# Kernel optimization log

Hardware: AMD Instinct MI355X
Metric: run time of the kernel (lower is better)

Reference implementation:

```python
import jax, jax.numpy as jnp
import numpy as np

DIM = 384
WIN = 7
HEADS = 12
N = WIN * WIN
B_ = 4096
NW = 64


def _relative_position_index(ws: int) -> np.ndarray:
    coords = np.stack(np.meshgrid(np.arange(ws), np.arange(ws), indexing='ij'))  # (2, ws, ws)
    flat = coords.reshape(2, -1)  # (2, N)
    rel = flat[:, :, None] - flat[:, None, :]  # (2, N, N)
    rel = rel.transpose(1, 2, 0).copy()  # (N, N, 2)
    rel[:, :, 0] += ws - 1
    rel[:, :, 1] += ws - 1
    rel[:, :, 0] *= 2 * ws - 1
    return rel.sum(-1).astype(np.int32)  # (N, N)


def setup_inputs() -> dict:
    key = jax.random.key(0)
    ks = jax.random.split(key, 6)
    x = jax.random.normal(ks[0], (B_, N, DIM), dtype=jnp.float32)
    mask = jnp.zeros((NW, N, N), dtype=jnp.float32)
    bias_table = 0.02 * jax.random.normal(ks[1], ((2 * WIN - 1) ** 2, HEADS), dtype=jnp.float32)
    qkv_w = jax.random.normal(ks[2], (3 * DIM, DIM), dtype=jnp.float32) / np.sqrt(DIM)
    qkv_b = jnp.zeros((3 * DIM,), dtype=jnp.float32)
    proj_w = jax.random.normal(ks[3], (DIM, DIM), dtype=jnp.float32) / np.sqrt(DIM)
    proj_b = jnp.zeros((DIM,), dtype=jnp.float32)
    rel_index = jnp.asarray(_relative_position_index(WIN))  # (N, N) int32
    return {"x": x, "mask": mask, "bias_table": bias_table, "qkv_w": qkv_w,
            "qkv_b": qkv_b, "proj_w": proj_w, "proj_b": proj_b, "rel_index": rel_index}


def reference(x, mask, bias_table, qkv_w, qkv_b, proj_w, proj_b, rel_index):
    Bw, n, c = x.shape
    h = bias_table.shape[1]
    d = c // h
    scale = d ** (-0.5)
    # qkv projection: (Bw, n, 3, h, d)
    qkv = (x @ qkv_w.T + qkv_b).reshape(Bw, n, 3, h, d)
    qkv = jnp.transpose(qkv, (2, 0, 3, 1, 4))  # (3, Bw, h, n, d)
    q, k, v = qkv[0], qkv[1], qkv[2]
    attn = jnp.einsum('bhqd,bhkd->bhqk', q * scale, k)  # (Bw, h, n, n)
    bias = bias_table[rel_index]  # (n, n, h)
    attn = attn + jnp.transpose(bias, (2, 0, 1))[None]  # broadcast over Bw
    nW = mask.shape[0]
    attn = attn.reshape(Bw // nW, nW, h, n, n) + mask[None, :, None]
    attn = attn.reshape(Bw, h, n, n)
    attn = jax.nn.softmax(attn, axis=-1)
    out = jnp.einsum('bhqk,bhkd->bhqd', attn, v)  # (Bw, h, n, d)
    out = jnp.transpose(out, (0, 2, 1, 3)).reshape(Bw, n, c)
    return out @ proj_w.T + proj_b
```

## Files before the change

### kernel.cpp

```cpp
#include <hip/hip_runtime.h>
#include <hip/hip_bf16.h>

#define DIM   384
#define NWIN  49
#define HEADS 12
#define SCALE 0.17677669529663687f

typedef unsigned short ushort;
using bf16x8 = __attribute__((ext_vector_type(8))) short;
using u16x4  = __attribute__((ext_vector_type(4))) ushort;
using f32x4  = __attribute__((ext_vector_type(4))) float;

__device__ __forceinline__ ushort f2bf(float f) {
  unsigned u = __float_as_uint(f);
  u += 0x7fff + ((u >> 16) & 1);
  return (ushort)(u >> 16);
}

typedef __attribute__((address_space(1))) const void gas_void;
typedef __attribute__((address_space(3))) void las_void;

__device__ __forceinline__ void gload16(const ushort* g, ushort* l) {
  __builtin_amdgcn_global_load_lds((gas_void*)g, (las_void*)l, 16, 0, 0);
}

__global__ void prep_kernel(const float* __restrict__ qkv_w, const float* __restrict__ proj_w,
                            const float* __restrict__ bias_table, const int* __restrict__ rel_index,
                            const float* __restrict__ mask, const float* __restrict__ qkv_b,
                            ushort* __restrict__ wqb, ushort* __restrict__ wpb,
                            float* __restrict__ qbF, float* __restrict__ bmF) {
  int i0 = blockIdx.x * 256 + threadIdx.x;
  int stride = gridDim.x * 256;
  for (int i = i0; i < 1152 * 384; i += stride) {
    float v = qkv_w[i];
    if (i < 384 * 384) v *= SCALE;
    wqb[i] = f2bf(v);
  }
  for (int i = i0; i < 384 * 384; i += stride) wpb[i] = f2bf(proj_w[i]);
  for (int i = i0; i < 1152; i += stride) qbF[i] = qkv_b[i] * (i < 384 ? SCALE : 1.f);
  for (int i = i0; i < 64 * HEADS * 4 * 4 * 64 * 4; i += stride) {
    int r = i & 3, lane = (i >> 2) & 63, kt = (i >> 8) & 3, wq = (i >> 10) & 3;
    int hw = i >> 12;
    int h = hw % HEADS, wdx = hw / HEADS;
    int q = wq * 16 + (lane >> 4) * 4 + r;
    int key = kt * 16 + (lane & 15);
    float v;
    if (q < NWIN)
      v = (key < NWIN) ? bias_table[rel_index[q * NWIN + key] * HEADS + h]
                         + mask[wdx * (NWIN * NWIN) + q * NWIN + key]
                       : -3.0e38f;
    else
      v = 0.f;
    bmF[i] = v;
  }
}

__global__ __launch_bounds__(256) void x2bf_kernel(const float* __restrict__ x,
                                                   ushort* __restrict__ xbf) {
  size_t i = (size_t)blockIdx.x * 256 + threadIdx.x;
  float4 f = ((const float4*)x)[i];
  u16x4 v4 = { f2bf(f.x), f2bf(f.y), f2bf(f.z), f2bf(f.w) };
  ((u16x4*)xbf)[i] = v4;
}

__global__ __launch_bounds__(256) void qkv_gemm_bf16_kernel(
    const ushort* __restrict__ xbf, const float* __restrict__ qbF,
    const ushort* __restrict__ wqb,
    ushort* __restrict__ qg, ushort* __restrict__ kg, ushort* __restrict__ vg)
{
  extern __shared__ ushort smA[];
  ushort* lA = smA;
  ushort* lB = smA + 16384;

  const int hw = blockIdx.x;
  const int xcd = hw & 7, slot = hw >> 3;
  const int pan = slot / 9, bN = slot - pan * 9;
  const int bM = (pan << 3) + xcd;
  const int m0 = bM * 128, n0 = bN * 128;
  const int which = bN / 3;
  ushort* outw = which == 0 ? qg : (which == 1 ? kg : vg);
  const int tid = threadIdx.x;
  const int w = tid >> 6, l = tid & 63;
  const int c = l & 15, g = l >> 4;
  const int wm = w >> 1, wn = w & 1;

  auto stageA = [&](int kc, int buf) {
    #pragma unroll
    for (int s = 0; s < 4; ++s) {
      int i = s * 256 + tid;
      int row = i >> 3, gc = i & 7;
      bf16x8 vx = *(const bf16x8*)(xbf + (size_t)(m0 + row) * DIM + kc * 64 + gc * 8);
      *(bf16x8*)&lA[buf * 8192 + row * 64 + ((gc ^ (row & 7)) << 3)] = vx;
    }
  };
  auto stageB = [&](int kc, int buf) {
    #pragma unroll
    for (int s = 0; s < 4; ++s) {
      int i = s * 256 + tid;
      int row = i >> 3, gc = i & 7;
      gload16(wqb + (size_t)(n0 + row) * DIM + kc * 64 + ((gc ^ (row & 7)) << 3),
              lB + buf * 8192 + i * 8);
    }
  };

  f32x4 acc[4][4] = {};
  stageA(0, 0); stageB(0, 0);
  stageA(1, 1); stageB(1, 1);
  __syncthreads();

  for (int kc = 0; kc < 6; ++kc) {
    const ushort* A = lA + (kc & 1) * 8192;
    const ushort* B = lB + (kc & 1) * 8192;
    #pragma unroll
    for (int kk = 0; kk < 2; ++kk) {
      int swz = ((kk * 4 + g) ^ (c & 7)) << 3;
      bf16x8 af[4], bfr[4];
      #pragma unroll
      for (int mt = 0; mt < 4; ++mt)
        af[mt] = *(const bf16x8*)&A[(wm * 64 + mt * 16 + c) * 64 + swz];
      #pragma unroll
      for (int nt = 0; nt < 4; ++nt)
        bfr[nt] = *(const bf16x8*)&B[(wn * 64 + nt * 16 + c) * 64 + swz];
      #pragma unroll
      for (int mt = 0; mt < 4; ++mt)
        #pragma unroll
        for (int nt = 0; nt < 4; ++nt)
          acc[mt][nt] = __builtin_amdgcn_mfma_f32_16x16x32_bf16(af[mt], bfr[nt], acc[mt][nt], 0, 0, 0);
    }
    __syncthreads();
    if (kc + 2 < 6) { stageA(kc + 2, kc & 1); stageB(kc + 2, kc & 1); }
  }

  #pragma unroll
  for (int nt = 0; nt < 4; ++nt) {
    int n = n0 + wn * 64 + nt * 16 + c;
    int h = (n - which * 384) >> 5;
    int d = n & 31;
    float qb_ = qbF[n];
    #pragma unroll
    for (int mt = 0; mt < 4; ++mt) {
      #pragma unroll
      for (int r = 0; r < 4; ++r) {
        int tok = m0 + wm * 64 + mt * 16 + g * 4 + r;
        int win = tok / 49;
        int tk = tok - win * 49;
        outw[((size_t)(win * HEADS + h) * NWIN + tk) * 32 + d] = f2bf(acc[mt][nt][r] + qb_);
      }
    }
  }
}

__global__ __launch_bounds__(256) void qkv_gemm_kernel(
    const float* __restrict__ x, const float* __restrict__ qbF,
    const ushort* __restrict__ wqb,
    ushort* __restrict__ qg, ushort* __restrict__ kg, ushort* __restrict__ vg)
{
  extern __shared__ ushort smA[];
  ushort* lA = smA;
  ushort* lB = smA + 16384;

  const int hw = blockIdx.x;
  const int xcd = hw & 7, slot = hw >> 3;
  const int pan = slot / 9, bN = slot - pan * 9;
  const int bM = (pan << 3) + xcd;
  const int m0 = bM * 128, n0 = bN * 128;
  const int which = bN / 3;
  ushort* outw = which == 0 ? qg : (which == 1 ? kg : vg);
  const int tid = threadIdx.x;
  const int w = tid >> 6, l = tid & 63;
  const int c = l & 15, g = l >> 4;
  const int wm = w >> 1, wn = w & 1;

  auto stageA = [&](int kc, int buf) {
    #pragma unroll
    for (int s = 0; s < 4; ++s) {
      int i = s * 256 + tid;
      int row = i >> 3, gc = i & 7;
      const float4* src = (const float4*)(x + (size_t)(m0 + row) * DIM + kc * 64 + gc * 8);
      float4 f0 = src[0], f1 = src[1];
      ushort tmp[8] = { f2bf(f0.x), f2bf(f0.y), f2bf(f0.z), f2bf(f0.w),
                        f2bf(f1.x), f2bf(f1.y), f2bf(f1.z), f2bf(f1.w) };
      *(bf16x8*)&lA[buf * 8192 + row * 64 + ((gc ^ (row & 7)) << 3)] = *(bf16x8*)tmp;
    }
  };
  auto stageB = [&](int kc, int buf) {
    #pragma unroll
    for (int s = 0; s < 4; ++s) {
      int i = s * 256 + tid;
      int row = i >> 3, gc = i & 7;
      gload16(wqb + (size_t)(n0 + row) * DIM + kc * 64 + ((gc ^ (row & 7)) << 3),
              lB + buf * 8192 + i * 8);
    }
  };

  f32x4 acc[4][4] = {};
  stageA(0, 0); stageB(0, 0);
  stageA(1, 1); stageB(1, 1);
  __syncthreads();

  for (int kc = 0; kc < 6; ++kc) {
    const ushort* A = lA + (kc & 1) * 8192;
    const ushort* B = lB + (kc & 1) * 8192;
    #pragma unroll
    for (int kk = 0; kk < 2; ++kk) {
      int swz = ((kk * 4 + g) ^ (c & 7)) << 3;
      bf16x8 af[4], bfr[4];
      #pragma unroll
      for (int mt = 0; mt < 4; ++mt)
        af[mt] = *(const bf16x8*)&A[(wm * 64 + mt * 16 + c) * 64 + swz];
      #pragma unroll
      for (int nt = 0; nt < 4; ++nt)
        bfr[nt] = *(const bf16x8*)&B[(wn * 64 + nt * 16 + c) * 64 + swz];
      #pragma unroll
      for (int mt = 0; mt < 4; ++mt)
        #pragma unroll
        for (int nt = 0; nt < 4; ++nt)
          acc[mt][nt] = __builtin_amdgcn_mfma_f32_16x16x32_bf16(af[mt], bfr[nt], acc[mt][nt], 0, 0, 0);
    }
    __syncthreads();
    if (kc + 2 < 6) { stageA(kc + 2, kc & 1); stageB(kc + 2, kc & 1); }
  }

  #pragma unroll
  for (int nt = 0; nt < 4; ++nt) {
    int n = n0 + wn * 64 + nt * 16 + c;
    int h = (n - which * 384) >> 5;
    int d = n & 31;
    float qb_ = qbF[n];
    #pragma unroll
    for (int mt = 0; mt < 4; ++mt) {
      #pragma unroll
      for (int r = 0; r < 4; ++r) {
        int tok = m0 + wm * 64 + mt * 16 + g * 4 + r;
        int win = tok / 49;
        int tk = tok - win * 49;
        outw[((size_t)(win * HEADS + h) * NWIN + tk) * 32 + d] = f2bf(acc[mt][nt][r] + qb_);
      }
    }
  }
}

#define VSTR 68
__global__ __launch_bounds__(256) void attn_kernel(
    const ushort* __restrict__ kg, const ushort* __restrict__ vg,
    const float* __restrict__ bmF, ushort* __restrict__ qg)
{
  __shared__ ushort vts[4][32 * VSTR];
  __shared__ ushort pbs[4][16 * 36];

  const int tid = threadIdx.x;
  const int w = tid >> 6, l = tid & 63;
  const int c = l & 15, g = l >> 4;
  const int task = blockIdx.x * 4 + w;
  const int win = task / 12, h = task - win * 12;
  const int wdx = win & 63;
  const float LOG2E = 1.4426950408889634f;

  const size_t sb = (size_t)(win * HEADS + h) * (NWIN * 32);
  ushort* qslice = qg + sb;
  const ushort* kb = kg + sb;
  const ushort* vb = vg + sb;
  ushort* vt = vts[w];
  ushort* pb = pbs[w];

  bf16x8 qf[4], kf[4];
  #pragma unroll
  for (int t = 0; t < 4; ++t) {
    qf[t] = *(const bf16x8*)(qslice + (t * 16 + c) * 32 + g * 8);
    kf[t] = *(const bf16x8*)(kb + (t * 16 + c) * 32 + g * 8);
  }
  #pragma unroll
  for (int it = 0; it < 25; ++it) {
    int i = it * 64 + l;
    if (i < NWIN * 32) vt[(i & 31) * VSTR + (i >> 5)] = vb[i];
  }
  for (int i = l; i < 32 * 15; i += 64) {
    int d = i / 15, t = NWIN + (i - d * 15);
    vt[d * VSTR + t] = 0;
  }

  const float* bmBase = bmF + (size_t)((wdx * HEADS + h) * 4) * 1024 + l * 4;

  #pragma unroll
  for (int qt = 0; qt < 4; ++qt) {
    f32x4 sacc[4] = {};
    #pragma unroll
    for (int kt = 0; kt < 4; ++kt)
      sacc[kt] = __builtin_amdgcn_mfma_f32_16x16x32_bf16(qf[qt], kf[kt], sacc[kt], 0, 0, 0);
    const f32x4* bw4 = (const f32x4*)(bmBase + qt * 1024);
    float p[4][4];
    {
      f32x4 b0 = bw4[0], b1 = bw4[64], b2 = bw4[128], b3 = bw4[192];
      #pragma unroll
      for (int r = 0; r < 4; ++r) {
        float s0 = sacc[0][r] + b0[r], s1 = sacc[1][r] + b1[r];
        float s2 = sacc[2][r] + b2[r], s3 = sacc[3][r] + b3[r];
        float mx = fmaxf(fmaxf(s0, s1), fmaxf(s2, s3));
        mx = fmaxf(mx, __shfl_xor(mx, 1, 64));
        mx = fmaxf(mx, __shfl_xor(mx, 2, 64));
        mx = fmaxf(mx, __shfl_xor(mx, 4, 64));
        mx = fmaxf(mx, __shfl_xor(mx, 8, 64));
        float p0 = __builtin_exp2f((s0 - mx) * LOG2E);
        float p1 = __builtin_exp2f((s1 - mx) * LOG2E);
        float p2 = __builtin_exp2f((s2 - mx) * LOG2E);
        float p3 = __builtin_exp2f((s3 - mx) * LOG2E);
        float sum = p0 + p1 + p2 + p3;
        sum += __shfl_xor(sum, 1, 64);
        sum += __shfl_xor(sum, 2, 64);
        sum += __shfl_xor(sum, 4, 64);
        sum += __shfl_xor(sum, 8, 64);
        float inv = 1.0f / sum;
        p[0][r] = p0 * inv; p[1][r] = p1 * inv; p[2][r] = p2 * inv; p[3][r] = p3 * inv;
      }
    }
    f32x4 pacc[2] = {};
    #pragma unroll
    for (int kkh = 0; kkh < 2; ++kkh) {
      #pragma unroll
      for (int t = 0; t < 2; ++t) {
        int kt = kkh * 2 + t;
        #pragma unroll
        for (int r = 0; r < 4; ++r)
          pb[(g * 4 + r) * 36 + t * 16 + c] = f2bf(p[kt][r]);
      }
      bf16x8 ap = *(const bf16x8*)&pb[c * 36 + g * 8];
      #pragma unroll
      for (int dt = 0; dt < 2; ++dt) {
        bf16x8 bv = *(const bf16x8*)&vt[(dt * 16 + c) * VSTR + kkh * 32 + g * 8];
        pacc[dt] = __builtin_amdgcn_mfma_f32_16x16x32_bf16(ap, bv, pacc[dt], 0, 0, 0);
      }
    }
    #pragma unroll
    for (int dt = 0; dt < 2; ++dt) {
      #pragma unroll
      for (int rr = 0; rr < 4; ++rr) {
        int tok = qt * 16 + g * 4 + rr;
        if (tok < NWIN)
          qslice[tok * 32 + dt * 16 + c] = f2bf(pacc[dt][rr]);
      }
    }
  }
}

__global__ __launch_bounds__(256, 2) void proj_kernel(
    const ushort* __restrict__ ao, const ushort* __restrict__ wpb,
    const float* __restrict__ proj_b, float* __restrict__ out)
{
  extern __shared__ ushort sm3[];
  ushort* lA = sm3;
  ushort* lB = sm3 + 16384;

  const int hw = blockIdx.x;
  const int xcd = hw & 7, slot = hw >> 3;
  const int pan = slot / 3, bN = slot - pan * 3;
  const int bM = (pan << 3) + xcd;
  const int m0 = bM * 128, n0 = bN * 128;
  const int tid = threadIdx.x;
  const int w = tid >> 6, l = tid & 63;
  const int c = l & 15, g = l >> 4;
  const int wm = w >> 1, wn = w & 1;

  auto stageA = [&](int kc, int buf) {
    #pragma unroll
    for (int s = 0; s < 4; ++s) {
      int i = s * 256 + tid;
      int row = i >> 3, gc = i & 7;
      int tok = m0 + row;
      int win = tok / 49;
      int tk = tok - win * 49;
      int sg = gc ^ (row & 7);
      int kfull = kc * 64 + sg * 8;
      gload16(ao + ((size_t)(win * HEADS + (kfull >> 5)) * NWIN + tk) * 32 + (kfull & 31),
              lA + buf * 8192 + i * 8);
    }
  };
  auto stageB = [&](int kc, int buf) {
    #pragma unroll
    for (int s = 0; s < 4; ++s) {
      int i = s * 256 + tid;
      int row = i >> 3, gc = i & 7;
      gload16(wpb + (size_t)(n0 + row) * DIM + kc * 64 + ((gc ^ (row & 7)) << 3),
              lB + buf * 8192 + i * 8);
    }
  };

  f32x4 acc[4][4] = {};
  stageA(0, 0); stageB(0, 0);
  stageA(1, 1); stageB(1, 1);
  __syncthreads();

  for (int kc = 0; kc < 6; ++kc) {
    const ushort* A = lA + (kc & 1) * 8192;
    const ushort* B = lB + (kc & 1) * 8192;
    #pragma unroll
    for (int kk = 0; kk < 2; ++kk) {
      int swz = ((kk * 4 + g) ^ (c & 7)) << 3;
      bf16x8 af[4], bfr[4];
      #pragma unroll
      for (int mt = 0; mt < 4; ++mt)
        af[mt] = *(const bf16x8*)&A[(wm * 64 + mt * 16 + c) * 64 + swz];
      #pragma unroll
      for (int nt = 0; nt < 4; ++nt)
        bfr[nt] = *(const bf16x8*)&B[(wn * 64 + nt * 16 + c) * 64 + swz];
      #pragma unroll
      for (int mt = 0; mt < 4; ++mt)
        #pragma unroll
        for (int nt = 0; nt < 4; ++nt)
          acc[mt][nt] = __builtin_amdgcn_mfma_f32_16x16x32_bf16(af[mt], bfr[nt], acc[mt][nt], 0, 0, 0);
    }
    __syncthreads();
    if (kc + 2 < 6) { stageA(kc + 2, kc & 1); stageB(kc + 2, kc & 1); }
  }

  #pragma unroll
  for (int nt = 0; nt < 4; ++nt) {
    int col = n0 + wn * 64 + nt * 16 + c;
    float pb = proj_b[col];
    #pragma unroll
    for (int mt = 0; mt < 4; ++mt) {
      #pragma unroll
      for (int r = 0; r < 4; ++r) {
        int row = m0 + wm * 64 + mt * 16 + g * 4 + r;
        out[(size_t)row * DIM + col] = acc[mt][nt][r] + pb;
      }
    }
  }
}

#define FWB_OFF 0
#define FQS_OFF 24576
#define FKS_OFF 29696
#define FVT_OFF 34816
#define FAO_OFF 39424
#define FSMEM_US 77056

__global__ __launch_bounds__(512, 2) void winattn_fused(
    const float* __restrict__ x, const float* __restrict__ qbF,
    const float* __restrict__ proj_b, const ushort* __restrict__ wqb,
    const ushort* __restrict__ wpb, const float* __restrict__ bmF,
    float* __restrict__ out)
{
  extern __shared__ ushort smem[];
  ushort* wb = smem + FWB_OFF;
  ushort* ao = smem + FAO_OFF;

  const int blk = blockIdx.x;
  const int tid = threadIdx.x;
  const int w = tid >> 6, l = tid & 63;
  const int c = l & 15, g = l >> 4;
  const int wm = w >> 1, wn = w & 1;
  const int win = w >> 2, wq = w & 3;
  const float LOG2E = 1.4426950408889634f;

  ushort* qsw = smem + FQS_OFF + win * 2560;
  ushort* ksw = smem + FKS_OFF + win * 2560;
  ushort* vtw = smem + FVT_OFF + win * 2304;
  ushort* psw = qsw;

  auto stage_qkv = [&](int h, int kc, int buf) {
    #pragma unroll
    for (int s = 0; s < 3; ++s) {
      int i = s * 512 + tid;
      int n = i >> 4, g16 = i & 15;
      int grow = (n >> 5) * 384 + h * 32 + (n & 31);
      int sg = (g16 & 8) | ((g16 & 7) ^ (n & 7));
      gload16(wqb + (size_t)grow * DIM + kc * 128 + (sg << 3), wb + buf * 12288 + i * 8);
    }
  };
  auto stage_proj = [&](int nb, int kc, int buf) {
    #pragma unroll
    for (int s = 0; s < 3; ++s) {
      int i = s * 512 + tid;
      int n = i >> 4, g16 = i & 15;
      int grow = nb * 96 + n;
      int sg = (g16 & 8) | ((g16 & 7) ^ (n & 7));
      gload16(wpb + (size_t)grow * DIM + kc * 128 + (sg << 3), wb + buf * 12288 + i * 8);
    }
  };

  bf16x8 areg[2][12] = {};
  auto compute_qkv = [&](int kcC, int buf, f32x4 (&acc)[2][3]) {
    const ushort* wcb = wb + buf * 12288;
    #pragma unroll
    for (int kk = 0; kk < 4; ++kk) {
      int sB = ((kk * 4 + g) ^ (c & 7)) << 3;
      #pragma unroll
      for (int nt = 0; nt < 3; ++nt) {
        int n = (wn * 3 + nt) * 16 + c;
        bf16x8 bb = *(const bf16x8*)&wcb[n * 128 + sB];
        acc[0][nt] = __builtin_amdgcn_mfma_f32_16x16x32_bf16(areg[0][kcC * 4 + kk], bb, acc[0][nt], 0, 0, 0);
        acc[1][nt] = __builtin_amdgcn_mfma_f32_16x16x32_bf16(areg[1][kcC * 4 + kk], bb, acc[1][nt], 0, 0, 0);
      }
    }
  };
  auto compute_proj = [&](int kcC, int buf, f32x4 (&acc)[2][3]) {
    const ushort* wcb = wb + buf * 12288;
    int r0 = wm * 32 + c;      if (r0 >= 98) r0 -= 64;
    int r1 = wm * 32 + 16 + c; if (r1 >= 98) r1 -= 64;
    #pragma unroll
    for (int kk = 0; kk < 4; ++kk) {
      int p = kcC * 16 + kk * 4 + g;
      int sw = (p ^ (c & 7)) << 3;
      bf16x8 a0 = *(const bf16x8*)&ao[r0 * 384 + sw];
      bf16x8 a1 = *(const bf16x8*)&ao[r1 * 384 + sw];
      int sB = ((kk * 4 + g) ^ (c & 7)) << 3;
      #pragma unroll
      for (int nt = 0; nt < 3; ++nt) {
        int n = (wn * 3 + nt) * 16 + c;
        bf16x8 bb = *(const bf16x8*)&wcb[n * 128 + sB];
        acc[0][nt] = __builtin_amdgcn_mfma_f32_16x16x32_bf16(a0, bb, acc[0][nt], 0, 0, 0);
        acc[1][nt] = __builtin_amdgcn_mfma_f32_16x16x32_bf16(a1, bb, acc[1][nt], 0, 0, 0);
      }
    }
  };

  stage_qkv(0, 0, 0);
  stage_qkv(0, 1, 1);
  {
    const float* xb = x + (size_t)blk * (2 * NWIN * DIM);
    for (int i = tid; i < 9408; i += 512) {
      float4 f = ((const float4*)xb)[i];
      int row = i / 96, c4 = i - row * 96;
      int k = c4 * 4;
      int gr = k >> 3;
      u16x4 v4 = { f2bf(f.x), f2bf(f.y), f2bf(f.z), f2bf(f.w) };
      *(u16x4*)&ao[row * 384 + ((gr ^ (row & 7)) << 3) + (k & 7)] = v4;
    }
  }
  __syncthreads();
  #pragma unroll
  for (int mt = 0; mt < 2; ++mt) {
    int row = wm * 32 + mt * 16 + c;
    int wi = row >> 6, tok = row & 63;
    if (tok < NWIN) {
      int ar = wi * 49 + tok;
      #pragma unroll
      for (int kg = 0; kg < 12; ++kg)
        areg[mt][kg] = *(const bf16x8*)&ao[ar * 384 + (((kg * 4 + g) ^ (ar & 7)) << 3)];
    }
  }

  for (int h = 0; h < HEADS; ++h) {
    f32x4 acc[2][3] = {};
    const int par = h & 1;
    compute_qkv(0, par, acc);
    __syncthreads();
    stage_qkv(h, 2, par);
    compute_qkv(1, par ^ 1, acc);
    __syncthreads();
    if (h < 11) stage_qkv(h + 1, 0, par ^ 1); else stage_proj(0, 0, par ^ 1);
    compute_qkv(2, par, acc);
    __syncthreads();
    if (h < 11) stage_qkv(h + 1, 1, par); else stage_proj(0, 1, par);
    {
      int winE = wm >> 1;
      ushort* qsE = smem + FQS_OFF + winE * 2560;
      ushort* ksE = smem + FKS_OFF + winE * 2560;
      ushort* vtE = smem + FVT_OFF + winE * 2304;
      #pragma unroll
      for (int nt = 0; nt < 3; ++nt) {
        int gnt = wn * 3 + nt;
        int which = gnt >> 1;
        int d = (gnt & 1) * 16 + c;
        float qb_ = qbF[which * 384 + h * 32 + d];
        #pragma unroll
        for (int mt = 0; mt < 2; ++mt) {
          #pragma unroll
          for (int r = 0; r < 4; ++r) {
            int tok = (wm & 1) * 32 + mt * 16 + g * 4 + r;
            float v = acc[mt][nt][r] + qb_;
            if (which == 0)      qsE[tok * 40 + d] = f2bf(v);
            else if (which == 1) ksE[tok * 40 + d] = f2bf(v);
            else                 vtE[d * 72 + tok] = f2bf(v);
          }
        }
      }
    }
    __syncthreads();

    const int wdx = ((blk << 1) + win) & 63;
    const f32x4* bw4 = (const f32x4*)(bmF + ((((size_t)(wdx * HEADS + h)) * 4 + wq) * 4 * 64 + l) * 4);
    f32x4 bmv[4];
    #pragma unroll
    for (int kt = 0; kt < 4; ++kt) bmv[kt] = bw4[kt * 64];

    f32x4 sacc[4] = {};
    {
      bf16x8 aq = *(const bf16x8*)&qsw[(wq * 16 + c) * 40 + g * 8];
      #pragma unroll
      for (int kt = 0; kt < 4; ++kt) {
        bf16x8 bk = *(const bf16x8*)&ksw[(kt * 16 + c) * 40 + g * 8];
        sacc[kt] = __builtin_amdgcn_mfma_f32_16x16x32_bf16(aq, bk, sacc[kt], 0, 0, 0);
      }
    }
    float p[4][4];
    #pragma unroll
    for (int r = 0; r < 4; ++r) {
      float s0 = sacc[0][r] + bmv[0][r], s1 = sacc[1][r] + bmv[1][r];
      float s2 = sacc[2][r] + bmv[2][r], s3 = sacc[3][r] + bmv[3][r];
      float mx = fmaxf(fmaxf(s0, s1), fmaxf(s2, s3));
      mx = fmaxf(mx, __shfl_xor(mx, 1, 64));
      mx = fmaxf(mx, __shfl_xor(mx, 2, 64));
      mx = fmaxf(mx, __shfl_xor(mx, 4, 64));
      mx = fmaxf(mx, __shfl_xor(mx, 8, 64));
      float p0 = __builtin_exp2f((s0 - mx) * LOG2E);
      float p1 = __builtin_exp2f((s1 - mx) * LOG2E);
      float p2 = __builtin_exp2f((s2 - mx) * LOG2E);
      float p3 = __builtin_exp2f((s3 - mx) * LOG2E);
      float sum = p0 + p1 + p2 + p3;
      sum += __shfl_xor(sum, 1, 64);
      sum += __shfl_xor(sum, 2, 64);
      sum += __shfl_xor(sum, 4, 64);
      sum += __shfl_xor(sum, 8, 64);
      float inv = 1.0f / sum;
      p[0][r] = p0 * inv; p[1][r] = p1 * inv; p[2][r] = p2 * inv; p[3][r] = p3 * inv;
    }
    f32x4 pacc2[2] = {};
    #pragma unroll
    for (int kkh = 0; kkh < 2; ++kkh) {
      #pragma unroll
      for (int t = 0; t < 2; ++t) {
        int kt = kkh * 2 + t;
        #pragma unroll
        for (int r = 0; r < 4; ++r)
          psw[(wq * 16 + g * 4 + r) * 40 + t * 16 + c] = f2bf(p[kt][r]);
      }
      bf16x8 ap = *(const bf16x8*)&psw[(wq * 16 + c) * 40 + g * 8];
      #pragma unroll
      for (int dt = 0; dt < 2; ++dt) {
        bf16x8 bv = *(const bf16x8*)&vtw[(dt * 16 + c) * 72 + kkh * 32 + g * 8];
        pacc2[dt] = __builtin_amdgcn_mfma_f32_16x16x32_bf16(ap, bv, pacc2[dt], 0, 0, 0);
      }
    }
    #pragma unroll
    for (int dt = 0; dt < 2; ++dt) {
      int gr0 = h * 4 + dt * 2 + (c >> 3);
      #pragma unroll
      for (int rr = 0; rr < 4; ++rr) {
        int tok = wq * 16 + g * 4 + rr;
        int row0 = win * 49 + tok;
        if (tok < NWIN)
          ao[row0 * 384 + (((gr0 ^ (row0 & 7)) << 3) | (c & 7))] = f2bf(pacc2[dt][rr]);
      }
    }
    __syncthreads();
  }

  __syncthreads();
  for (int nb = 0; nb < 4; ++nb) {
    f32x4 acc[2][3] = {};
    const int pb0 = (nb * 3) & 1;
    compute_proj(0, pb0, acc);
    __syncthreads();
    stage_proj(nb, 2, pb0);
    compute_proj(1, pb0 ^ 1, acc);
    __syncthreads();
    if (nb < 3) stage_proj(nb + 1, 0, pb0 ^ 1);
    compute_proj(2, pb0, acc);
    __syncthreads();
    if (nb < 3) stage_proj(nb + 1, 1, pb0);
    #pragma unroll
    for (int nt = 0; nt < 3; ++nt) {
      int col = nb * 96 + (wn * 3 + nt) * 16 + c;
      float pb = proj_b[col];
      #pragma unroll
      for (int mt = 0; mt < 2; ++mt) {
        #pragma unroll
        for (int r = 0; r < 4; ++r) {
          int mrow = wm * 32 + mt * 16 + g * 4 + r;
          if (mrow < 98) {
            int wi = mrow >= NWIN;
            int tok = mrow - (wi ? NWIN : 0);
            out[((size_t)((blk << 1) + wi) * NWIN + tok) * DIM + col] = acc[mt][nt][r] + pb;
          }
        }
      }
    }
  }
}

extern "C" void kernel_launch(void* const* d_in, const int* in_sizes, int n_in,
                              void* d_out, int out_size, void* d_ws, size_t ws_size,
                              hipStream_t stream) {
  const float* x          = (const float*)d_in[0];
  const float* mask       = (const float*)d_in[1];
  const float* bias_table = (const float*)d_in[2];
  const float* qkv_w      = (const float*)d_in[3];
  const float* qkv_b      = (const float*)d_in[4];
  const float* proj_w     = (const float*)d_in[5];
  const float* proj_b     = (const float*)d_in[6];
  const int*   rel_index  = (const int*)d_in[7];
  float* out = (float*)d_out;

  ushort* wqb = (ushort*)d_ws;
  ushort* wpb = (ushort*)((char*)d_ws + 884736);
  float*  qbF = (float*)((char*)d_ws + 1179648);
  float*  bmF = (float*)((char*)d_ws + 1184256);
  ushort* qg  = (ushort*)((char*)d_ws + 13767168);
  ushort* kg  = (ushort*)((char*)d_ws + 167907840);
  ushort* vg  = (ushort*)((char*)d_ws + 322048512);
  ushort* xbf = (ushort*)((char*)d_ws + 476189184);
  const size_t NEED1 = 630329856ull;
  const size_t NEED2 = 476189184ull;

  prep_kernel<<<1024, 256, 0, stream>>>(qkv_w, proj_w, bias_table, rel_index, mask, qkv_b,
                                        wqb, wpb, qbF, bmF);

  if (ws_size >= NEED1) {
    x2bf_kernel<<<75264, 256, 0, stream>>>(x, xbf);
    hipFuncSetAttribute((const void*)qkv_gemm_bf16_kernel,
                        hipFuncAttributeMaxDynamicSharedMemorySize, 65536);
    qkv_gemm_bf16_kernel<<<14112, 256, 65536, stream>>>(xbf, qbF, wqb, qg, kg, vg);
    attn_kernel<<<12288, 256, 0, stream>>>(kg, vg, bmF, qg);
    hipFuncSetAttribute((const void*)proj_kernel,
                        hipFuncAttributeMaxDynamicSharedMemorySize, 65536);
    proj_kernel<<<4704, 256, 65536, stream>>>(qg, wpb, proj_b, out);
  } else if (ws_size >= NEED2) {
    hipFuncSetAttribute((const void*)qkv_gemm_kernel,
                        hipFuncAttributeMaxDynamicSharedMemorySize, 65536);
    qkv_gemm_kernel<<<14112, 256, 65536, stream>>>(x, qbF, wqb, qg, kg, vg);
    attn_kernel<<<12288, 256, 0, stream>>>(kg, vg, bmF, qg);
    hipFuncSetAttribute((const void*)proj_kernel,
                        hipFuncAttributeMaxDynamicSharedMemorySize, 65536);
    proj_kernel<<<4704, 256, 65536, stream>>>(qg, wpb, proj_b, out);
  } else {
    hipFuncSetAttribute((const void*)winattn_fused,
                        hipFuncAttributeMaxDynamicSharedMemorySize, FSMEM_US * 2);
    winattn_fused<<<2048, 512, FSMEM_US * 2, stream>>>(x, qbF, proj_b, wqb, wpb, bmF, out);
  }
}
```

Baseline: 794.6 us.

## Use 64-row GEMM tiles with A held in registers for QKV and proj

Replaces the 128x128 QKV and projection GEMM kernels with 64x128 tile variants that load each wave's A rows (the full K=384) directly from global memory into registers. Only B (the weights) is staged through LDS, so LDS drops to 32KB of static shared memory. The intent is to raise occupancy, double the number of blocks, and remove the A-staging LDS round trip. The cost is more register pressure from holding 24 bf16x8 vectors per lane, and the weight tiles are re-read twice as often across blocks.

```diff
diff --git a/kernel.cpp b/kernel.cpp
--- a/kernel.cpp
+++ b/kernel.cpp
@@ -63,20 +63,18 @@
   ((u16x4*)xbf)[i] = v4;
 }
 
-__global__ __launch_bounds__(256) void qkv_gemm_bf16_kernel(
+__global__ __launch_bounds__(256) void qkv64_kernel(
     const ushort* __restrict__ xbf, const float* __restrict__ qbF,
     const ushort* __restrict__ wqb,
     ushort* __restrict__ qg, ushort* __restrict__ kg, ushort* __restrict__ vg)
 {
-  extern __shared__ ushort smA[];
-  ushort* lA = smA;
-  ushort* lB = smA + 16384;
+  __shared__ ushort lB[2 * 8192];
 
   const int hw = blockIdx.x;
   const int xcd = hw & 7, slot = hw >> 3;
   const int pan = slot / 9, bN = slot - pan * 9;
-  const int bM = (pan << 3) + xcd;
-  const int m0 = bM * 128, n0 = bN * 128;
+  const int bM = pan * 8 + xcd;
+  const int m0 = bM * 64, n0 = bN * 128;
   const int which = bN / 3;
   ushort* outw = which == 0 ? qg : (which == 1 ? kg : vg);
   const int tid = threadIdx.x;
@@ -84,15 +82,6 @@
   const int c = l & 15, g = l >> 4;
   const int wm = w >> 1, wn = w & 1;
 
-  auto stageA = [&](int kc, int buf) {
-    #pragma unroll
-    for (int s = 0; s < 4; ++s) {
-      int i = s * 256 + tid;
-      int row = i >> 3, gc = i & 7;
-      bf16x8 vx = *(const bf16x8*)(xbf + (size_t)(m0 + row) * DIM + kc * 64 + gc * 8);
-      *(bf16x8*)&lA[buf * 8192 + row * 64 + ((gc ^ (row & 7)) << 3)] = vx;
-    }
-  };
   auto stageB = [&](int kc, int buf) {
     #pragma unroll
     for (int s = 0; s < 4; ++s) {
@@ -103,32 +92,37 @@
     }
   };
 
-  f32x4 acc[4][4] = {};
-  stageA(0, 0); stageB(0, 0);
-  stageA(1, 1); stageB(1, 1);
+  bf16x8 areg[2][12];
+  #pragma unroll
+  for (int mt = 0; mt < 2; ++mt) {
+    const ushort* ar = xbf + (size_t)(m0 + wm * 32 + mt * 16 + c) * DIM + g * 8;
+    #pragma unroll
+    for (int j = 0; j < 12; ++j)
+      areg[mt][j] = *(const bf16x8*)(ar + j * 32);
+  }
+
+  f32x4 acc[2][4] = {};
+  stageB(0, 0);
+  stageB(1, 1);
   __syncthreads();
 
   for (int kc = 0; kc < 6; ++kc) {
-    const ushort* A = lA + (kc & 1) * 8192;
     const ushort* B = lB + (kc & 1) * 8192;
     #pragma unroll
     for (int kk = 0; kk < 2; ++kk) {
       int swz = ((kk * 4 + g) ^ (c & 7)) << 3;
-      bf16x8 af[4], bfr[4];
-      #pragma unroll
-      for (int mt = 0; mt < 4; ++mt)
-        af[mt] = *(const bf16x8*)&A[(wm * 64 + mt * 16 + c) * 64 + swz];
+      bf16x8 bfr[4];
       #pragma unroll
       for (int nt = 0; nt < 4; ++nt)
         bfr[nt] = *(const bf16x8*)&B[(wn * 64 + nt * 16 + c) * 64 + swz];
       #pragma unroll
-      for (int mt = 0; mt < 4; ++mt)
+      for (int mt = 0; mt < 2; ++mt)
         #pragma unroll
         for (int nt = 0; nt < 4; ++nt)
-          acc[mt][nt] = __builtin_amdgcn_mfma_f32_16x16x32_bf16(af[mt], bfr[nt], acc[mt][nt], 0, 0, 0);
-    }
-    __syncthreads();
-    if (kc + 2 < 6) { stageA(kc + 2, kc & 1); stageB(kc + 2, kc & 1); }
+          acc[mt][nt] = __builtin_amdgcn_mfma_f32_16x16x32_bf16(areg[mt][kc * 2 + kk], bfr[nt], acc[mt][nt], 0, 0, 0);
+    }
+    __syncthreads();
+    if (kc + 2 < 6) stageB(kc + 2, kc & 1);
   }
 
   #pragma unroll
@@ -138,13 +132,89 @@
     int d = n & 31;
     float qb_ = qbF[n];
     #pragma unroll
-    for (int mt = 0; mt < 4; ++mt) {
+    for (int mt = 0; mt < 2; ++mt) {
       #pragma unroll
       for (int r = 0; r < 4; ++r) {
-        int tok = m0 + wm * 64 + mt * 16 + g * 4 + r;
+        int tok = m0 + wm * 32 + mt * 16 + g * 4 + r;
         int win = tok / 49;
         int tk = tok - win * 49;
         outw[((size_t)(win * HEADS + h) * NWIN + tk) * 32 + d] = f2bf(acc[mt][nt][r] + qb_);
+      }
+    }
+  }
+}
+
+__global__ __launch_bounds__(256) void proj64_kernel(
+    const ushort* __restrict__ ao, const ushort* __restrict__ wpb,
+    const float* __restrict__ proj_b, float* __restrict__ out)
+{
+  __shared__ ushort lB[2 * 8192];
+
+  const int hw = blockIdx.x;
+  const int xcd = hw & 7, slot = hw >> 3;
+  const int pan = slot / 3, bN = slot - pan * 3;
+  const int bM = pan * 8 + xcd;
+  const int m0 = bM * 64, n0 = bN * 128;
+  const int tid = threadIdx.x;
+  const int w = tid >> 6, l = tid & 63;
+  const int c = l & 15, g = l >> 4;
+  const int wm = w >> 1, wn = w & 1;
+
+  auto stageB = [&](int kc, int buf) {
+    #pragma unroll
+    for (int s = 0; s < 4; ++s) {
+      int i = s * 256 + tid;
+      int row = i >> 3, gc = i & 7;
+      gload16(wpb + (size_t)(n0 + row) * DIM + kc * 64 + ((gc ^ (row & 7)) << 3),
+              lB + buf * 8192 + i * 8);
+    }
+  };
+
+  bf16x8 areg[2][12];
+  #pragma unroll
+  for (int mt = 0; mt < 2; ++mt) {
+    int row = m0 + wm * 32 + mt * 16 + c;
+    int win = row / 49, tk = row - win * 49;
+    const ushort* ab = ao + ((size_t)win * HEADS * NWIN + tk) * 32 + g * 8;
+    #pragma unroll
+    for (int j = 0; j < 12; ++j)
+      areg[mt][j] = *(const bf16x8*)(ab + (size_t)j * (NWIN * 32));
+  }
+
+  f32x4 acc[2][4] = {};
+  stageB(0, 0);
+  stageB(1, 1);
+  __syncthreads();
+
+  for (int kc = 0; kc < 6; ++kc) {
+    const ushort* B = lB + (kc & 1) * 8192;
+    #pragma unroll
+    for (int kk = 0; kk < 2; ++kk) {
+      int swz = ((kk * 4 + g) ^ (c & 7)) << 3;
+      bf16x8 bfr[4];
+      #pragma unroll
+      for (int nt = 0; nt < 4; ++nt)
+        bfr[nt] = *(const bf16x8*)&B[(wn * 64 + nt * 16 + c) * 64 + swz];
+      #pragma unroll
+      for (int mt = 0; mt < 2; ++mt)
+        #pragma unroll
+        for (int nt = 0; nt < 4; ++nt)
+          acc[mt][nt] = __builtin_amdgcn_mfma_f32_16x16x32_bf16(areg[mt][kc * 2 + kk], bfr[nt], acc[mt][nt], 0, 0, 0);
+    }
+    __syncthreads();
+    if (kc + 2 < 6) stageB(kc + 2, kc & 1);
+  }
+
+  #pragma unroll
+  for (int nt = 0; nt < 4; ++nt) {
+    int col = n0 + wn * 64 + nt * 16 + c;
+    float pb = proj_b[col];
+    #pragma unroll
+    for (int mt = 0; mt < 2; ++mt) {
+      #pragma unroll
+      for (int r = 0; r < 4; ++r) {
+        int row = m0 + wm * 32 + mt * 16 + g * 4 + r;
+        out[(size_t)row * DIM + col] = acc[mt][nt][r] + pb;
       }
     }
   }
@@ -708,13 +778,9 @@
 
   if (ws_size >= NEED1) {
     x2bf_kernel<<<75264, 256, 0, stream>>>(x, xbf);
-    hipFuncSetAttribute((const void*)qkv_gemm_bf16_kernel,
-                        hipFuncAttributeMaxDynamicSharedMemorySize, 65536);
-    qkv_gemm_bf16_kernel<<<14112, 256, 65536, stream>>>(xbf, qbF, wqb, qg, kg, vg);
+    qkv64_kernel<<<28224, 256, 0, stream>>>(xbf, qbF, wqb, qg, kg, vg);
     attn_kernel<<<12288, 256, 0, stream>>>(kg, vg, bmF, qg);
-    hipFuncSetAttribute((const void*)proj_kernel,
-                        hipFuncAttributeMaxDynamicSharedMemorySize, 65536);
-    proj_kernel<<<4704, 256, 65536, stream>>>(qg, wpb, proj_b, out);
+    proj64_kernel<<<9408, 256, 0, stream>>>(qg, wpb, proj_b, out);
   } else if (ws_size >= NEED2) {
     hipFuncSetAttribute((const void*)qkv_gemm_kernel,
                         hipFuncAttributeMaxDynamicSharedMemorySize, 65536);
```

New measurement: 1.007 ms. 1.27x slower.
